# Kernel optimization log

Measured on AMD Instinct MI355X. Metric: run time of the kernel, lower is better.

Reference implementation:

```python
import jax, jax.numpy as jnp
import numpy as np

NUM_OBJECTS = 6          # self.NUM_OBJECTS
SCORE_THRESH = 1e-4      # self.score_tresh
NMS_THRESHS = jnp.asarray(np.arange(0.001, 1.0, 0.1), dtype=jnp.float32)  # 10 thresholds
K_CAND = 1024            # fixed-shape cap on (proposal,class) candidates per image
CLASS_OFFSET = 4096.0    # > max image coord; batched_nms per-class offset trick


def _iou_matrix(b):
    # b: [K,4] xyxy -> [K,K] IoU
    x1, y1, x2, y2 = b[:, 0], b[:, 1], b[:, 2], b[:, 3]
    area = (x2 - x1) * (y2 - y1)
    iw = jnp.clip(jnp.minimum(x2[:, None], x2[None, :]) - jnp.maximum(x1[:, None], x1[None, :]), 0.0)
    ih = jnp.clip(jnp.minimum(y2[:, None], y2[None, :]) - jnp.maximum(y1[:, None], y1[None, :]), 0.0)
    inter = iw * ih
    union = area[:, None] + area[None, :] - inter
    return jnp.where(union > 0, inter / union, 0.0)


def _greedy_nms(iou, valid, thresh):
    # candidates are pre-sorted by descending score; sequential greedy suppression
    K = valid.shape[0]
    ar = jnp.arange(K)
    def body(i, keep):
        sup = keep[i] & (iou[i] > thresh) & (ar > i)
        return keep & ~sup
    return jax.lax.fori_loop(0, K, body, valid)


def _per_image(logits, boxes, feats, hw):
    # logits [N,81], boxes [N,80,4], feats [N,2048], hw [2] (h,w)
    C = boxes.shape[1]
    probs = jax.nn.softmax(logits, axis=-1)[:, :C]          # drop background class
    h = hw[0].astype(boxes.dtype)
    w = hw[1].astype(boxes.dtype)
    b = jnp.stack([jnp.clip(boxes[..., 0], 0.0, w),         # clip to image
                   jnp.clip(boxes[..., 1], 0.0, h),
                   jnp.clip(boxes[..., 2], 0.0, w),
                   jnp.clip(boxes[..., 3], 0.0, h)], axis=-1)
    scores = probs.reshape(-1)                              # [N*C]
    vals, idx = jax.lax.top_k(jnp.where(scores > SCORE_THRESH, scores, -1.0), K_CAND)
    cand_valid = vals > SCORE_THRESH
    cb = b.reshape(-1, 4)[idx]                              # [K,4]
    cls = (idx % C).astype(boxes.dtype)
    prop = idx // C                                         # proposal row index
    iou = _iou_matrix(cb + cls[:, None] * CLASS_OFFSET)     # per-class NMS via offsets
    keeps = jax.vmap(lambda t: _greedy_nms(iou, cand_valid, t))(NMS_THRESHS)  # [T,K]
    counts = keeps.sum(axis=1)
    # torch loop: break at first (smallest) thresh yielding len(ids)==6, i.e. >=6 kept
    ok = counts >= NUM_OBJECTS
    t_sel = jnp.where(jnp.any(ok), jnp.argmax(ok), NMS_THRESHS.shape[0] - 1)
    keep = keeps[t_sel]
    _, top = jax.lax.top_k(jnp.where(keep, vals, -jnp.inf), NUM_OBJECTS)
    ids = prop[top]                                         # [6]
    return feats[ids].T                                     # [2048, 6] (permute(1,0))


def _forward(cls_logits, boxes, feature_pooled, image_hw):
    return jax.vmap(_per_image)(cls_logits, boxes, feature_pooled, image_hw)  # [B,2048,6]


def setup_inputs() -> dict:
    key = jax.random.key(0)
    k1, k2, k3, k4, k5 = jax.random.split(key, 5)
    B, N, C, D = 8, 1000, 80, 2048
    cls_logits = jax.random.normal(k1, (B, N, C + 1), dtype=jnp.float32)
    ctr = jax.random.uniform(k2, (B, N, C, 2), minval=0.0, maxval=800.0)
    sz = jax.random.uniform(k3, (B, N, C, 2), minval=8.0, maxval=200.0)
    boxes = jnp.concatenate([ctr - sz * 0.5, ctr + sz * 0.5], axis=-1).astype(jnp.float32)
    feature_pooled = jax.random.normal(k4, (B, N, D), dtype=jnp.float32)
    image_hw = jax.random.randint(k5, (B, 2), 600, 800, dtype=jnp.int32)
    return {"cls_logits": cls_logits, "boxes": boxes,
            "feature_pooled": feature_pooled, "image_hw": image_hw}


def reference(cls_logits, boxes, feature_pooled, image_hw):
    return _forward(cls_logits, boxes, feature_pooled, image_hw)
```

## Files before the change

kernel.cpp:

```cpp
#include <hip/hip_runtime.h>
#include <cmath>
#include <cstdint>

#define NB 8
#define NPROP 1000
#define NCLS 80
#define NLOG 81
#define KCAND 1024
#define NTH 10
#define DFEAT 2048
#define NOBJ 6
#define NSCORE (NPROP*NCLS)
#define HBLK 8
#define HCHUNK (NSCORE/HBLK)
#define PCHUNK (NPROP/HBLK)
#define CCAP 64

constexpr size_t OFF_SCORES = 0;
constexpr size_t SZ_SCORES  = (size_t)NB * NSCORE * 4;
constexpr size_t OFF_LISTA  = OFF_SCORES + SZ_SCORES;
constexpr size_t SZ_LISTA   = (size_t)NB * 20 * KCAND * 8;
constexpr size_t OFF_H1     = OFF_LISTA;
constexpr size_t OFF_H2     = OFF_H1 + (size_t)NB * HBLK * 2048 * 4;
constexpr size_t OFF_PIV    = OFF_H2 + (size_t)NB * HBLK * 2048 * 4;
constexpr size_t OFF_CBUF   = OFF_PIV + (size_t)NB * 8 * 4;
constexpr size_t OFF_CANDK  = OFF_LISTA + SZ_LISTA;
constexpr size_t SZ_CANDK   = (size_t)NB * KCAND * 8;
constexpr size_t OFF_CX1    = OFF_CANDK + SZ_CANDK;
constexpr size_t SZ_CARR    = (size_t)NB * KCAND * 4;
constexpr size_t OFF_CY1    = OFF_CX1 + SZ_CARR;
constexpr size_t OFF_CX2    = OFF_CY1 + SZ_CARR;
constexpr size_t OFF_CY2    = OFF_CX2 + SZ_CARR;
constexpr size_t OFF_CAREA  = OFF_CY2 + SZ_CARR;
constexpr size_t OFF_CPROP  = OFF_CAREA + SZ_CARR;
constexpr size_t OFF_VALIDW = OFF_CPROP + SZ_CARR;
constexpr size_t SZ_VALIDW  = (size_t)NB * 16 * 8;
constexpr size_t OFF_CCNT   = OFF_VALIDW + SZ_VALIDW;
constexpr size_t OFF_CLIST  = OFF_CCNT + (size_t)NB * NCLS * 4;
constexpr size_t OFF_KEEPS  = OFF_CLIST + (size_t)NB * NCLS * CCAP * 4;
constexpr size_t SZ_KEEPS   = (size_t)NB * NTH * 16 * 8;

__device__ __forceinline__ float nms_th(int t) {
    return (float)(0.001 + 0.1 * (double)t);
}

__device__ __forceinline__ unsigned score_vkey(float v) {
    float vv = (v > 1e-4f) ? v : -1.0f;
    unsigned bits = __float_as_uint(vv);
    unsigned u = (bits & 0x80000000u) ? ~bits : (bits | 0x80000000u);
    return ~u;
}

__global__ __launch_bounds__(1024) void k_softhist(const float* __restrict__ logits,
                                                   float* __restrict__ scores,
                                                   unsigned* __restrict__ hist1) {
    __shared__ unsigned hh[2048];
    int img = blockIdx.x >> 3, blk = blockIdx.x & 7;
    int tid = threadIdx.x, wid = tid >> 6, lane = tid & 63;
    hh[tid] = 0; hh[tid + 1024] = 0;
    __syncthreads();
    for (int p = wid; p < PCHUNK; p += 16) {
        int prop = blk * PCHUNK + p;
        const float* L = logits + ((size_t)img * NPROP + prop) * NLOG;
        float l0 = L[lane];
        float l1 = (lane < 17) ? L[64 + lane] : -INFINITY;
        float m = fmaxf(l0, l1);
        #pragma unroll
        for (int o = 32; o > 0; o >>= 1) m = fmaxf(m, __shfl_xor(m, o, 64));
        float e0 = expf(l0 - m);
        float e1 = (lane < 17) ? expf(l1 - m) : 0.f;
        float s = e0 + e1;
        #pragma unroll
        for (int o = 32; o > 0; o >>= 1) s += __shfl_xor(s, o, 64);
        float* op = scores + ((size_t)img * NPROP + prop) * NCLS;
        float p0 = e0 / s;
        op[lane] = p0;
        atomicAdd(&hh[score_vkey(p0) >> 21], 1u);
        if (lane < 16) {
            float p1 = e1 / s;
            op[64 + lane] = p1;
            atomicAdd(&hh[score_vkey(p1) >> 21], 1u);
        }
    }
    __syncthreads();
    unsigned* outp = hist1 + ((size_t)img * HBLK + blk) * 2048;
    outp[tid] = hh[tid];
    outp[tid + 1024] = hh[tid + 1024];
}

__device__ __forceinline__ void pivot_scan(const unsigned* __restrict__ h8, unsigned K,
                                           int* __restrict__ out_b, int* __restrict__ out_rem) {
    __shared__ unsigned wsum[16];
    int tid = threadIdx.x;
    unsigned a = 0, b = 0;
    #pragma unroll
    for (int s = 0; s < HBLK; ++s) {
        a += h8[s * 2048 + 2 * tid];
        b += h8[s * 2048 + 2 * tid + 1];
    }
    unsigned p = a + b;
    unsigned x = p;
    #pragma unroll
    for (int d = 1; d < 64; d <<= 1) {
        unsigned y = __shfl_up(x, (unsigned)d, 64);
        if ((tid & 63) >= d) x += y;
    }
    if ((tid & 63) == 63) wsum[tid >> 6] = x;
    __syncthreads();
    if (tid < 16) {
        unsigned w = wsum[tid];
        #pragma unroll
        for (int d = 1; d < 16; d <<= 1) {
            unsigned y = __shfl_up(w, (unsigned)d, 64);
            if (tid >= d) w += y;
        }
        wsum[tid] = w;
    }
    __syncthreads();
    unsigned wex = (tid >= 64) ? wsum[(tid >> 6) - 1] : 0u;
    unsigned incl = x + wex;
    unsigned E = incl - p;
    if (E < K && E + a >= K)              { *out_b = 2 * tid;     *out_rem = (int)(K - E); }
    else if (E + a < K && E + a + b >= K) { *out_b = 2 * tid + 1; *out_rem = (int)(K - (E + a)); }
}

__global__ __launch_bounds__(1024) void k_hist2p(const float* __restrict__ scores,
                                                 const unsigned* __restrict__ hist1,
                                                 unsigned* __restrict__ hist2,
                                                 int* __restrict__ piv) {
    __shared__ unsigned hh[2048];
    __shared__ int sb, sr;
    int img = blockIdx.x >> 3, blk = blockIdx.x & 7;
    int tid = threadIdx.x;
    hh[tid] = 0; hh[tid + 1024] = 0;
    pivot_scan(hist1 + (size_t)img * HBLK * 2048, KCAND, &sb, &sr);
    __syncthreads();
    unsigned b1 = (unsigned)sb;
    const float* sc = scores + (size_t)img * NSCORE + (size_t)blk * HCHUNK;
    for (int e = tid; e < HCHUNK; e += 1024) {
        unsigned vk = score_vkey(sc[e]);
        if ((vk >> 21) == b1) atomicAdd(&hh[(vk >> 10) & 2047u], 1u);
    }
    __syncthreads();
    unsigned* outp = hist2 + ((size_t)img * HBLK + blk) * 2048;
    outp[tid] = hh[tid];
    outp[tid + 1024] = hh[tid + 1024];
    if (blk == 0 && tid == 0) {
        piv[img * 8 + 0] = sb;
        piv[img * 8 + 1] = sr;
        piv[img * 8 + 3] = 0;
    }
}

__global__ __launch_bounds__(1024) void k_gatherp(const float* __restrict__ scores,
                                                  const unsigned* __restrict__ hist2,
                                                  int* __restrict__ piv,
                                                  unsigned long long* __restrict__ cbuf,
                                                  int* __restrict__ ccnt,
                                                  unsigned long long* __restrict__ validw,
                                                  unsigned long long* __restrict__ keeps) {
    __shared__ int sb2, sr2;
    __shared__ unsigned lcnt, gbase;
    int img = blockIdx.x >> 3, blk = blockIdx.x & 7;
    int tid = threadIdx.x;
    if (blockIdx.x == 0) {
        if (tid < NB * NCLS) ccnt[tid] = 0;
        if (tid >= 640 && tid < 640 + NB * 16) validw[tid - 640] = 0ULL;
    }
    if (blockIdx.x == 1) {
        for (int k = tid; k < NB * NTH * 16; k += 1024) keeps[k] = 0ULL;
    }
    if (tid == 0) lcnt = 0;
    unsigned K2 = (unsigned)piv[img * 8 + 1];
    pivot_scan(hist2 + (size_t)img * HBLK * 2048, K2, &sb2, &sr2);
    __syncthreads();
    unsigned T22 = ((unsigned)piv[img * 8 + 0] << 11) | (unsigned)sb2;
    const float* sc = scores + (size_t)img * NSCORE + (size_t)blk * HCHUNK;
    unsigned long long sel[(HCHUNK + 1023) / 1024];
    int ns = 0;
    for (int e = tid; e < HCHUNK; e += 1024) {
        unsigned vk = score_vkey(sc[e]);
        if ((vk >> 10) <= T22)
            sel[ns++] = ((unsigned long long)vk << 32) | (unsigned)(blk * HCHUNK + e);
    }
    unsigned lp = atomicAdd(&lcnt, (unsigned)ns);
    __syncthreads();
    if (tid == 0) gbase = atomicAdd((unsigned*)&piv[img * 8 + 3], lcnt);
    __syncthreads();
    unsigned long long* ob = cbuf + (size_t)img * 2048;
    for (int i = 0; i < ns; ++i) {
        unsigned pos = gbase + lp + (unsigned)i;
        if (pos < 2048) ob[pos] = sel[i];
    }
}

__global__ __launch_bounds__(256) void k_rankcand(const unsigned long long* __restrict__ cbuf,
                                                  const int* __restrict__ piv,
                                                  const float* __restrict__ boxes,
                                                  const int* __restrict__ hw,
                                                  float* __restrict__ cx1, float* __restrict__ cy1,
                                                  float* __restrict__ cx2, float* __restrict__ cy2,
                                                  float* __restrict__ car, int* __restrict__ cprop,
                                                  unsigned long long* __restrict__ validw,
                                                  int* __restrict__ ccnt, int* __restrict__ clist) {
    __shared__ unsigned long long keys[2048];
    int img = blockIdx.x >> 3, sl = blockIdx.x & 7;
    int tid = threadIdx.x;
    int cnt = piv[img * 8 + 3]; if (cnt > 2048) cnt = 2048;
    const unsigned long long* ib = cbuf + (size_t)img * 2048;
    #pragma unroll
    for (int k = 0; k < 8; ++k) {
        int t = k * 256 + tid;
        keys[t] = (t < cnt) ? ib[t] : ~0ULL;
    }
    __syncthreads();
    unsigned long long a = keys[sl * 256 + tid];
    int r = 0;
    #pragma unroll 8
    for (int j = 0; j < cnt; ++j) r += (keys[j] < a) ? 1 : 0;
    if (sl * 256 + tid < cnt && r < KCAND) {
        unsigned u   = ~(unsigned)(a >> 32);
        unsigned idx = (unsigned)a;
        const unsigned uth = __float_as_uint(1e-4f) | 0x80000000u;
        bool valid = u > uth;
        int prop = (int)(idx / NCLS);
        int cls  = (int)(idx - (unsigned)prop * NCLS);
        const float4 bx = *(const float4*)(boxes + ((((size_t)img * NPROP + prop) * NCLS + cls) << 2));
        float h = (float)hw[img * 2 + 0];
        float w = (float)hw[img * 2 + 1];
        float x1 = fminf(fmaxf(bx.x, 0.f), w);
        float y1 = fminf(fmaxf(bx.y, 0.f), h);
        float x2 = fminf(fmaxf(bx.z, 0.f), w);
        float y2 = fminf(fmaxf(bx.w, 0.f), h);
        float offc = __fmul_rn((float)cls, 4096.0f);
        x1 = __fadd_rn(x1, offc); y1 = __fadd_rn(y1, offc);
        x2 = __fadd_rn(x2, offc); y2 = __fadd_rn(y2, offc);
        float area = __fmul_rn(__fsub_rn(x2, x1), __fsub_rn(y2, y1));
        int o = img * KCAND + r;
        cx1[o] = x1; cy1[o] = y1; cx2[o] = x2; cy2[o] = y2;
        car[o] = area; cprop[o] = prop;
        if (valid) atomicOr(&validw[img * 16 + (r >> 6)], 1ULL << (r & 63));
        int slot = atomicAdd(&ccnt[img * NCLS + cls], 1);
        if (slot < CCAP) clist[(img * NCLS + cls) * CCAP + slot] = r;
    }
}

__global__ __launch_bounds__(256) void k_cnms(const int* __restrict__ ccnt,
                                              const int* __restrict__ clist,
                                              const float* __restrict__ cx1,
                                              const float* __restrict__ cy1,
                                              const float* __restrict__ cx2,
                                              const float* __restrict__ cy2,
                                              const float* __restrict__ car,
                                              const unsigned long long* __restrict__ validw,
                                              unsigned long long* __restrict__ keeps) {
    int gid  = blockIdx.x * 4 + (threadIdx.x >> 6);
    int lane = threadIdx.x & 63;
    if (gid >= NB * NCLS) return;
    int img = gid / NCLS, cls = gid - img * NCLS;
    int n = ccnt[img * NCLS + cls];
    if (n > CCAP) n = CCAP;
    if (n == 0) return;
    int r = (lane < n) ? clist[(img * NCLS + cls) * CCAP + lane] : 0x7fffffff;
    int pos = 0;
    for (int j = 0; j < n; ++j) {
        int rj = __shfl(r, j, 64);
        pos += (rj < r) ? 1 : 0;
    }
    int srt = 0;
    for (int j = 0; j < n; ++j) {
        int pj = __shfl(pos, j, 64);
        int rj = __shfl(r, j, 64);
        if (pj == lane) srt = rj;
    }
    bool act = lane < n;
    int base = img * KCAND;
    float x1 = 0, y1 = 0, x2 = 0, y2 = 0, ar = 0;
    bool val = false;
    if (act) {
        x1 = cx1[base + srt]; y1 = cy1[base + srt];
        x2 = cx2[base + srt]; y2 = cy2[base + srt]; ar = car[base + srt];
        val = (validw[img * 16 + (srt >> 6)] >> (srt & 63)) & 1ULL;
    }
    unsigned long long m[NTH];
    #pragma unroll
    for (int t = 0; t < NTH; ++t) m[t] = 0ULL;
    for (int b = 0; b < n; ++b) {
        float xj1 = __shfl(x1, b, 64), yj1 = __shfl(y1, b, 64);
        float xj2 = __shfl(x2, b, 64), yj2 = __shfl(y2, b, 64);
        float aj  = __shfl(ar, b, 64);
        float iw = fmaxf(__fsub_rn(fminf(x2, xj2), fmaxf(x1, xj1)), 0.f);
        float ih = fmaxf(__fsub_rn(fminf(y2, yj2), fmaxf(y1, yj1)), 0.f);
        float inter = __fmul_rn(iw, ih);
        float uni   = __fsub_rn(__fadd_rn(ar, aj), inter);
        float iou   = (uni > 0.f) ? __fdiv_rn(inter, uni) : 0.f;
        if (act && b < lane) {
            #pragma unroll
            for (int t = 0; t < NTH; ++t)
                if (iou > nms_th(t)) m[t] |= 1ULL << b;
        }
    }
    unsigned long long vmask = __ballot(act && val);
    for (int t = 0; t < NTH; ++t) {
        unsigned long long keep = vmask;
        for (int it = 0; it <= n; ++it) {
            bool nk = act && val && ((m[t] & keep) == 0ULL);
            unsigned long long nb = __ballot(nk);
            if (nb == keep) break;
            keep = nb;
        }
        if (act && ((keep >> lane) & 1ULL))
            atomicOr(&keeps[((size_t)img * NTH + t) * 16 + (srt >> 6)], 1ULL << (srt & 63));
    }
}

__global__ __launch_bounds__(256) void k_selfeat(const unsigned long long* __restrict__ keeps,
                                                 const int* __restrict__ cprop,
                                                 const float* __restrict__ feats,
                                                 float* __restrict__ outp) {
    __shared__ int scnt[NTH];
    __shared__ unsigned long long skw[16];
    __shared__ int stsel;
    __shared__ int sids[NOBJ];
    int img = blockIdx.x >> 3;
    int tid = threadIdx.x;
    if (tid < NTH) scnt[tid] = 0;
    __syncthreads();
    if (tid < NTH * 16) {
        unsigned long long w = keeps[(size_t)img * NTH * 16 + tid];
        int pc = __popcll(w);
        if (pc) atomicAdd(&scnt[tid >> 4], pc);
    }
    __syncthreads();
    if (tid == 0) {
        int tsel = NTH - 1;
        for (int t = 0; t < NTH; ++t) if (scnt[t] >= NOBJ) { tsel = t; break; }
        stsel = tsel;
    }
    __syncthreads();
    if (tid < 16) skw[tid] = keeps[((size_t)img * NTH + stsel) * 16 + tid];
    __syncthreads();
    if (tid == 0) {
        int got = 0;
        for (int k = 0; k < 16 && got < NOBJ; ++k) {
            unsigned long long x = skw[k];
            while (x && got < NOBJ) {
                int b = __builtin_ctzll(x);
                sids[got++] = cprop[img * KCAND + k * 64 + b];
                x &= x - 1;
            }
        }
        for (int k = 0; k < 16 && got < NOBJ; ++k) {
            unsigned long long x = ~skw[k];
            while (x && got < NOBJ) {
                int b = __builtin_ctzll(x);
                sids[got++] = cprop[img * KCAND + k * 64 + b];
                x &= x - 1;
            }
        }
    }
    __syncthreads();
    int d = (blockIdx.x & 7) * 256 + tid;
    const float* fb = feats + (size_t)img * NPROP * DFEAT;
    float* ob = outp + ((size_t)img * DFEAT + d) * NOBJ;
    #pragma unroll
    for (int s = 0; s < NOBJ; ++s)
        ob[s] = fb[(size_t)sids[s] * DFEAT + d];
}

extern "C" void kernel_launch(void* const* d_in, const int* in_sizes, int n_in,
                              void* d_out, int out_size, void* d_ws, size_t ws_size,
                              hipStream_t stream) {
    const float* logits = (const float*)d_in[0];
    const float* boxes  = (const float*)d_in[1];
    const float* feats  = (const float*)d_in[2];
    const int*   hw     = (const int*)d_in[3];
    float* outp = (float*)d_out;

    char* ws = (char*)d_ws;
    float*              scores = (float*)(ws + OFF_SCORES);
    unsigned*           hist1  = (unsigned*)(ws + OFF_H1);
    unsigned*           hist2  = (unsigned*)(ws + OFF_H2);
    int*                piv    = (int*)(ws + OFF_PIV);
    unsigned long long* cbuf   = (unsigned long long*)(ws + OFF_CBUF);
    float* cx1 = (float*)(ws + OFF_CX1);
    float* cy1 = (float*)(ws + OFF_CY1);
    float* cx2 = (float*)(ws + OFF_CX2);
    float* cy2 = (float*)(ws + OFF_CY2);
    float* car = (float*)(ws + OFF_CAREA);
    int*   cprop = (int*)(ws + OFF_CPROP);
    unsigned long long* validw = (unsigned long long*)(ws + OFF_VALIDW);
    int*   ccnt  = (int*)(ws + OFF_CCNT);
    int*   clist = (int*)(ws + OFF_CLIST);
    unsigned long long* keeps  = (unsigned long long*)(ws + OFF_KEEPS);

    k_softhist<<<NB * HBLK, 1024, 0, stream>>>(logits, scores, hist1);
    k_hist2p<<<NB * HBLK, 1024, 0, stream>>>(scores, hist1, hist2, piv);
    k_gatherp<<<NB * HBLK, 1024, 0, stream>>>(scores, hist2, piv, cbuf, ccnt, validw, keeps);
    k_rankcand<<<NB * HBLK, 256, 0, stream>>>(cbuf, piv, boxes, hw,
                                              cx1, cy1, cx2, cy2, car, cprop,
                                              validw, ccnt, clist);
    k_cnms<<<(NB * NCLS + 3) / 4, 256, 0, stream>>>(ccnt, clist, cx1, cy1, cx2, cy2,
                                                    car, validw, keeps);
    k_selfeat<<<NB * HBLK, 256, 0, stream>>>(keeps, cprop, feats, outp);
}
```

Measured before the change: 163.6 us.

## Fuse pivot, gather, sort, NMS and feature select into one per-image kernel

Five kernels after the softmax/histogram pass are merged into a single kernel with one 1024-thread block per image. Candidates, boxes, per-class lists and keep masks now live in shared memory, and the O(n^2) rank sort is replaced by an in-LDS bitonic sort of 2048 keys. The goal is to remove four launches and their global-memory round trips. In exchange, only 8 blocks run, so each block scans the whole 80000-score array twice, and every image's NMS and feature copy run serially within one CU.

```diff
diff --git a/kernel.cpp b/kernel.cpp
--- a/kernel.cpp
+++ b/kernel.cpp
@@ -12,33 +12,12 @@
 #define NOBJ 6
 #define NSCORE (NPROP*NCLS)
 #define HBLK 8
-#define HCHUNK (NSCORE/HBLK)
 #define PCHUNK (NPROP/HBLK)
 #define CCAP 64
 
 constexpr size_t OFF_SCORES = 0;
 constexpr size_t SZ_SCORES  = (size_t)NB * NSCORE * 4;
-constexpr size_t OFF_LISTA  = OFF_SCORES + SZ_SCORES;
-constexpr size_t SZ_LISTA   = (size_t)NB * 20 * KCAND * 8;
-constexpr size_t OFF_H1     = OFF_LISTA;
-constexpr size_t OFF_H2     = OFF_H1 + (size_t)NB * HBLK * 2048 * 4;
-constexpr size_t OFF_PIV    = OFF_H2 + (size_t)NB * HBLK * 2048 * 4;
-constexpr size_t OFF_CBUF   = OFF_PIV + (size_t)NB * 8 * 4;
-constexpr size_t OFF_CANDK  = OFF_LISTA + SZ_LISTA;
-constexpr size_t SZ_CANDK   = (size_t)NB * KCAND * 8;
-constexpr size_t OFF_CX1    = OFF_CANDK + SZ_CANDK;
-constexpr size_t SZ_CARR    = (size_t)NB * KCAND * 4;
-constexpr size_t OFF_CY1    = OFF_CX1 + SZ_CARR;
-constexpr size_t OFF_CX2    = OFF_CY1 + SZ_CARR;
-constexpr size_t OFF_CY2    = OFF_CX2 + SZ_CARR;
-constexpr size_t OFF_CAREA  = OFF_CY2 + SZ_CARR;
-constexpr size_t OFF_CPROP  = OFF_CAREA + SZ_CARR;
-constexpr size_t OFF_VALIDW = OFF_CPROP + SZ_CARR;
-constexpr size_t SZ_VALIDW  = (size_t)NB * 16 * 8;
-constexpr size_t OFF_CCNT   = OFF_VALIDW + SZ_VALIDW;
-constexpr size_t OFF_CLIST  = OFF_CCNT + (size_t)NB * NCLS * 4;
-constexpr size_t OFF_KEEPS  = OFF_CLIST + (size_t)NB * NCLS * CCAP * 4;
-constexpr size_t SZ_KEEPS   = (size_t)NB * NTH * 16 * 8;
+constexpr size_t OFF_H1     = OFF_SCORES + SZ_SCORES;
 
 __device__ __forceinline__ float nms_th(int t) {
     return (float)(0.001 + 0.1 * (double)t);
@@ -88,16 +67,11 @@
     outp[tid + 1024] = hh[tid + 1024];
 }
 
-__device__ __forceinline__ void pivot_scan(const unsigned* __restrict__ h8, unsigned K,
-                                           int* __restrict__ out_b, int* __restrict__ out_rem) {
-    __shared__ unsigned wsum[16];
+__device__ __forceinline__ void pivot_lds(const unsigned* __restrict__ h, unsigned K,
+                                          int* __restrict__ out_b, int* __restrict__ out_rem,
+                                          unsigned* __restrict__ wsum) {
     int tid = threadIdx.x;
-    unsigned a = 0, b = 0;
-    #pragma unroll
-    for (int s = 0; s < HBLK; ++s) {
-        a += h8[s * 2048 + 2 * tid];
-        b += h8[s * 2048 + 2 * tid + 1];
-    }
+    unsigned a = h[2 * tid], b = h[2 * tid + 1];
     unsigned p = a + b;
     unsigned x = p;
     #pragma unroll
@@ -118,217 +92,198 @@
     }
     __syncthreads();
     unsigned wex = (tid >= 64) ? wsum[(tid >> 6) - 1] : 0u;
-    unsigned incl = x + wex;
-    unsigned E = incl - p;
+    unsigned E = x + wex - p;
     if (E < K && E + a >= K)              { *out_b = 2 * tid;     *out_rem = (int)(K - E); }
     else if (E + a < K && E + a + b >= K) { *out_b = 2 * tid + 1; *out_rem = (int)(K - (E + a)); }
 }
 
-__global__ __launch_bounds__(1024) void k_hist2p(const float* __restrict__ scores,
-                                                 const unsigned* __restrict__ hist1,
-                                                 unsigned* __restrict__ hist2,
-                                                 int* __restrict__ piv) {
-    __shared__ unsigned hh[2048];
-    __shared__ int sb, sr;
-    int img = blockIdx.x >> 3, blk = blockIdx.x & 7;
-    int tid = threadIdx.x;
-    hh[tid] = 0; hh[tid + 1024] = 0;
-    pivot_scan(hist1 + (size_t)img * HBLK * 2048, KCAND, &sb, &sr);
-    __syncthreads();
-    unsigned b1 = (unsigned)sb;
-    const float* sc = scores + (size_t)img * NSCORE + (size_t)blk * HCHUNK;
-    for (int e = tid; e < HCHUNK; e += 1024) {
+__global__ __launch_bounds__(1024) void k_mega2(const float* __restrict__ scores,
+                                                const unsigned* __restrict__ hist1,
+                                                const float* __restrict__ boxes,
+                                                const int* __restrict__ hw,
+                                                const float* __restrict__ feats,
+                                                float* __restrict__ outp) {
+    __shared__ __align__(16) unsigned char smem[51200];
+    unsigned*           hist  = (unsigned*)(smem);
+    unsigned long long* keys  = (unsigned long long*)(smem);
+    int*                clist = (int*)(smem);
+    float* bx1 = (float*)(smem + 24576);
+    float* by1 = (float*)(smem + 28672);
+    float* bx2 = (float*)(smem + 32768);
+    float* by2 = (float*)(smem + 36864);
+    float* bar = (float*)(smem + 40960);
+    int*   bprop = (int*)(smem + 45056);
+    unsigned long long* bvalid = (unsigned long long*)(smem + 49152);
+    int*   ccnt  = (int*)(smem + 49280);
+    unsigned long long* keep10 = (unsigned long long*)(smem + 49600);
+    int*   scnt  = (int*)(smem + 50880);
+    __shared__ unsigned wsum[16];
+    __shared__ int sb1, sr1, sb2, sr2, stsel;
+    __shared__ int sids[NOBJ];
+    __shared__ unsigned scounter;
+
+    const int img = blockIdx.x;
+    const int tid = threadIdx.x;
+    const int wv  = tid >> 6, lane = tid & 63;
+    const float* sc = scores + (size_t)img * NSCORE;
+
+    {
+        const unsigned* h8 = hist1 + (size_t)img * HBLK * 2048;
+        unsigned s0 = 0, s1 = 0;
+        #pragma unroll
+        for (int s = 0; s < HBLK; ++s) {
+            s0 += h8[s * 2048 + tid];
+            s1 += h8[s * 2048 + tid + 1024];
+        }
+        hist[tid] = s0; hist[tid + 1024] = s1;
+    }
+    __syncthreads();
+    pivot_lds(hist, KCAND, &sb1, &sr1, wsum);
+    __syncthreads();
+    int b1 = sb1, rem1 = sr1;
+
+    hist[tid] = 0; hist[tid + 1024] = 0;
+    __syncthreads();
+    for (int e = tid; e < NSCORE; e += 1024) {
         unsigned vk = score_vkey(sc[e]);
-        if ((vk >> 21) == b1) atomicAdd(&hh[(vk >> 10) & 2047u], 1u);
-    }
-    __syncthreads();
-    unsigned* outp = hist2 + ((size_t)img * HBLK + blk) * 2048;
-    outp[tid] = hh[tid];
-    outp[tid + 1024] = hh[tid + 1024];
-    if (blk == 0 && tid == 0) {
-        piv[img * 8 + 0] = sb;
-        piv[img * 8 + 1] = sr;
-        piv[img * 8 + 3] = 0;
-    }
-}
-
-__global__ __launch_bounds__(1024) void k_gatherp(const float* __restrict__ scores,
-                                                  const unsigned* __restrict__ hist2,
-                                                  int* __restrict__ piv,
-                                                  unsigned long long* __restrict__ cbuf,
-                                                  int* __restrict__ ccnt,
-                                                  unsigned long long* __restrict__ validw,
-                                                  unsigned long long* __restrict__ keeps) {
-    __shared__ int sb2, sr2;
-    __shared__ unsigned lcnt, gbase;
-    int img = blockIdx.x >> 3, blk = blockIdx.x & 7;
-    int tid = threadIdx.x;
-    if (blockIdx.x == 0) {
-        if (tid < NB * NCLS) ccnt[tid] = 0;
-        if (tid >= 640 && tid < 640 + NB * 16) validw[tid - 640] = 0ULL;
-    }
-    if (blockIdx.x == 1) {
-        for (int k = tid; k < NB * NTH * 16; k += 1024) keeps[k] = 0ULL;
-    }
-    if (tid == 0) lcnt = 0;
-    unsigned K2 = (unsigned)piv[img * 8 + 1];
-    pivot_scan(hist2 + (size_t)img * HBLK * 2048, K2, &sb2, &sr2);
-    __syncthreads();
-    unsigned T22 = ((unsigned)piv[img * 8 + 0] << 11) | (unsigned)sb2;
-    const float* sc = scores + (size_t)img * NSCORE + (size_t)blk * HCHUNK;
-    unsigned long long sel[(HCHUNK + 1023) / 1024];
-    int ns = 0;
-    for (int e = tid; e < HCHUNK; e += 1024) {
+        if ((int)(vk >> 21) == b1) atomicAdd(&hist[(vk >> 10) & 2047u], 1u);
+    }
+    __syncthreads();
+    pivot_lds(hist, (unsigned)rem1, &sb2, &sr2, wsum);
+    __syncthreads();
+    unsigned T22 = ((unsigned)b1 << 11) | (unsigned)sb2;
+
+    __syncthreads();
+    keys[tid] = ~0ULL; keys[tid + 1024] = ~0ULL;
+    if (tid == 0) scounter = 0;
+    __syncthreads();
+    for (int e = tid; e < NSCORE; e += 1024) {
         unsigned vk = score_vkey(sc[e]);
-        if ((vk >> 10) <= T22)
-            sel[ns++] = ((unsigned long long)vk << 32) | (unsigned)(blk * HCHUNK + e);
-    }
-    unsigned lp = atomicAdd(&lcnt, (unsigned)ns);
-    __syncthreads();
-    if (tid == 0) gbase = atomicAdd((unsigned*)&piv[img * 8 + 3], lcnt);
-    __syncthreads();
-    unsigned long long* ob = cbuf + (size_t)img * 2048;
-    for (int i = 0; i < ns; ++i) {
-        unsigned pos = gbase + lp + (unsigned)i;
-        if (pos < 2048) ob[pos] = sel[i];
-    }
-}
-
-__global__ __launch_bounds__(256) void k_rankcand(const unsigned long long* __restrict__ cbuf,
-                                                  const int* __restrict__ piv,
-                                                  const float* __restrict__ boxes,
-                                                  const int* __restrict__ hw,
-                                                  float* __restrict__ cx1, float* __restrict__ cy1,
-                                                  float* __restrict__ cx2, float* __restrict__ cy2,
-                                                  float* __restrict__ car, int* __restrict__ cprop,
-                                                  unsigned long long* __restrict__ validw,
-                                                  int* __restrict__ ccnt, int* __restrict__ clist) {
-    __shared__ unsigned long long keys[2048];
-    int img = blockIdx.x >> 3, sl = blockIdx.x & 7;
-    int tid = threadIdx.x;
-    int cnt = piv[img * 8 + 3]; if (cnt > 2048) cnt = 2048;
-    const unsigned long long* ib = cbuf + (size_t)img * 2048;
-    #pragma unroll
-    for (int k = 0; k < 8; ++k) {
-        int t = k * 256 + tid;
-        keys[t] = (t < cnt) ? ib[t] : ~0ULL;
-    }
-    __syncthreads();
-    unsigned long long a = keys[sl * 256 + tid];
-    int r = 0;
-    #pragma unroll 8
-    for (int j = 0; j < cnt; ++j) r += (keys[j] < a) ? 1 : 0;
-    if (sl * 256 + tid < cnt && r < KCAND) {
-        unsigned u   = ~(unsigned)(a >> 32);
-        unsigned idx = (unsigned)a;
-        const unsigned uth = __float_as_uint(1e-4f) | 0x80000000u;
-        bool valid = u > uth;
-        int prop = (int)(idx / NCLS);
-        int cls  = (int)(idx - (unsigned)prop * NCLS);
-        const float4 bx = *(const float4*)(boxes + ((((size_t)img * NPROP + prop) * NCLS + cls) << 2));
-        float h = (float)hw[img * 2 + 0];
-        float w = (float)hw[img * 2 + 1];
-        float x1 = fminf(fmaxf(bx.x, 0.f), w);
-        float y1 = fminf(fmaxf(bx.y, 0.f), h);
-        float x2 = fminf(fmaxf(bx.z, 0.f), w);
-        float y2 = fminf(fmaxf(bx.w, 0.f), h);
-        float offc = __fmul_rn((float)cls, 4096.0f);
-        x1 = __fadd_rn(x1, offc); y1 = __fadd_rn(y1, offc);
-        x2 = __fadd_rn(x2, offc); y2 = __fadd_rn(y2, offc);
-        float area = __fmul_rn(__fsub_rn(x2, x1), __fsub_rn(y2, y1));
-        int o = img * KCAND + r;
-        cx1[o] = x1; cy1[o] = y1; cx2[o] = x2; cy2[o] = y2;
-        car[o] = area; cprop[o] = prop;
-        if (valid) atomicOr(&validw[img * 16 + (r >> 6)], 1ULL << (r & 63));
-        int slot = atomicAdd(&ccnt[img * NCLS + cls], 1);
-        if (slot < CCAP) clist[(img * NCLS + cls) * CCAP + slot] = r;
-    }
-}
-
-__global__ __launch_bounds__(256) void k_cnms(const int* __restrict__ ccnt,
-                                              const int* __restrict__ clist,
-                                              const float* __restrict__ cx1,
-                                              const float* __restrict__ cy1,
-                                              const float* __restrict__ cx2,
-                                              const float* __restrict__ cy2,
-                                              const float* __restrict__ car,
-                                              const unsigned long long* __restrict__ validw,
-                                              unsigned long long* __restrict__ keeps) {
-    int gid  = blockIdx.x * 4 + (threadIdx.x >> 6);
-    int lane = threadIdx.x & 63;
-    if (gid >= NB * NCLS) return;
-    int img = gid / NCLS, cls = gid - img * NCLS;
-    int n = ccnt[img * NCLS + cls];
-    if (n > CCAP) n = CCAP;
-    if (n == 0) return;
-    int r = (lane < n) ? clist[(img * NCLS + cls) * CCAP + lane] : 0x7fffffff;
-    int pos = 0;
-    for (int j = 0; j < n; ++j) {
-        int rj = __shfl(r, j, 64);
-        pos += (rj < r) ? 1 : 0;
-    }
-    int srt = 0;
-    for (int j = 0; j < n; ++j) {
-        int pj = __shfl(pos, j, 64);
-        int rj = __shfl(r, j, 64);
-        if (pj == lane) srt = rj;
-    }
-    bool act = lane < n;
-    int base = img * KCAND;
-    float x1 = 0, y1 = 0, x2 = 0, y2 = 0, ar = 0;
-    bool val = false;
-    if (act) {
-        x1 = cx1[base + srt]; y1 = cy1[base + srt];
-        x2 = cx2[base + srt]; y2 = cy2[base + srt]; ar = car[base + srt];
-        val = (validw[img * 16 + (srt >> 6)] >> (srt & 63)) & 1ULL;
-    }
-    unsigned long long m[NTH];
-    #pragma unroll
-    for (int t = 0; t < NTH; ++t) m[t] = 0ULL;
-    for (int b = 0; b < n; ++b) {
-        float xj1 = __shfl(x1, b, 64), yj1 = __shfl(y1, b, 64);
-        float xj2 = __shfl(x2, b, 64), yj2 = __shfl(y2, b, 64);
-        float aj  = __shfl(ar, b, 64);
-        float iw = fmaxf(__fsub_rn(fminf(x2, xj2), fmaxf(x1, xj1)), 0.f);
-        float ih = fmaxf(__fsub_rn(fminf(y2, yj2), fmaxf(y1, yj1)), 0.f);
-        float inter = __fmul_rn(iw, ih);
-        float uni   = __fsub_rn(__fadd_rn(ar, aj), inter);
-        float iou   = (uni > 0.f) ? __fdiv_rn(inter, uni) : 0.f;
-        if (act && b < lane) {
+        if ((vk >> 10) <= T22) {
+            unsigned pos = atomicAdd(&scounter, 1u);
+            if (pos < 2048) keys[pos] = ((unsigned long long)vk << 32) | (unsigned)e;
+        }
+    }
+    __syncthreads();
+    int cnt = (int)scounter; if (cnt > 2048) cnt = 2048;
+
+    for (int k = 2; k <= 2048; k <<= 1) {
+        for (int j = k >> 1; j > 0; j >>= 1) {
             #pragma unroll
-            for (int t = 0; t < NTH; ++t)
-                if (iou > nms_th(t)) m[t] |= 1ULL << b;
-        }
-    }
-    unsigned long long vmask = __ballot(act && val);
-    for (int t = 0; t < NTH; ++t) {
-        unsigned long long keep = vmask;
-        for (int it = 0; it <= n; ++it) {
-            bool nk = act && val && ((m[t] & keep) == 0ULL);
-            unsigned long long nb = __ballot(nk);
-            if (nb == keep) break;
-            keep = nb;
-        }
-        if (act && ((keep >> lane) & 1ULL))
-            atomicOr(&keeps[((size_t)img * NTH + t) * 16 + (srt >> 6)], 1ULL << (srt & 63));
-    }
-}
-
-__global__ __launch_bounds__(256) void k_selfeat(const unsigned long long* __restrict__ keeps,
-                                                 const int* __restrict__ cprop,
-                                                 const float* __restrict__ feats,
-                                                 float* __restrict__ outp) {
-    __shared__ int scnt[NTH];
-    __shared__ unsigned long long skw[16];
-    __shared__ int stsel;
-    __shared__ int sids[NOBJ];
-    int img = blockIdx.x >> 3;
-    int tid = threadIdx.x;
+            for (int s = 0; s < 2; ++s) {
+                int i = s * 1024 + tid;
+                int ixj = i ^ j;
+                if (ixj > i) {
+                    bool up = ((i & k) == 0);
+                    unsigned long long a = keys[i], b = keys[ixj];
+                    if ((a > b) == up) { keys[i] = b; keys[ixj] = a; }
+                }
+            }
+            __syncthreads();
+        }
+    }
+
+    int mycls = -1;
+    {
+        bool have = (tid < KCAND) && (tid < cnt);
+        unsigned long long a = have ? keys[tid] : ~0ULL;
+        bool valid = false;
+        if (have) {
+            unsigned u   = ~(unsigned)(a >> 32);
+            unsigned idx = (unsigned)a;
+            const unsigned uth = __float_as_uint(1e-4f) | 0x80000000u;
+            valid = u > uth;
+            int prop = (int)(idx / NCLS);
+            int cls  = (int)(idx - (unsigned)prop * NCLS);
+            mycls = cls;
+            const float4 bx = *(const float4*)(boxes + ((((size_t)img * NPROP + prop) * NCLS + cls) << 2));
+            float h = (float)hw[img * 2 + 0];
+            float w = (float)hw[img * 2 + 1];
+            float x1 = fminf(fmaxf(bx.x, 0.f), w);
+            float y1 = fminf(fmaxf(bx.y, 0.f), h);
+            float x2 = fminf(fmaxf(bx.z, 0.f), w);
+            float y2 = fminf(fmaxf(bx.w, 0.f), h);
+            float offc = __fmul_rn((float)cls, 4096.0f);
+            x1 = __fadd_rn(x1, offc); y1 = __fadd_rn(y1, offc);
+            x2 = __fadd_rn(x2, offc); y2 = __fadd_rn(y2, offc);
+            float area = __fmul_rn(__fsub_rn(x2, x1), __fsub_rn(y2, y1));
+            bx1[tid] = x1; by1[tid] = y1; bx2[tid] = x2; by2[tid] = y2;
+            bar[tid] = area; bprop[tid] = prop;
+        }
+        unsigned long long bal = __ballot(valid);
+        if (tid < KCAND && lane == 0) bvalid[wv] = bal;
+    }
+    __syncthreads();
+
+    if (tid < NCLS) ccnt[tid] = 0;
+    if (tid < NTH * 16) keep10[tid] = 0ULL;
+    __syncthreads();
+    if (mycls >= 0) {
+        int slot = atomicAdd(&ccnt[mycls], 1);
+        if (slot < CCAP) clist[mycls * CCAP + slot] = tid;
+    }
+    __syncthreads();
+
+    for (int cl = wv; cl < NCLS; cl += 16) {
+        int n = ccnt[cl];
+        if (n > CCAP) n = CCAP;
+        if (n == 0) continue;
+        int r = (lane < n) ? clist[cl * CCAP + lane] : 0x7fffffff;
+        int pos = 0;
+        for (int j = 0; j < n; ++j) {
+            int rj = __shfl(r, j, 64);
+            pos += (rj < r) ? 1 : 0;
+        }
+        int srt = 0;
+        for (int j = 0; j < n; ++j) {
+            int pj = __shfl(pos, j, 64);
+            int rj = __shfl(r, j, 64);
+            if (pj == lane) srt = rj;
+        }
+        bool act = lane < n;
+        float x1 = 0, y1 = 0, x2 = 0, y2 = 0, ar = 0;
+        bool val = false;
+        if (act) {
+            x1 = bx1[srt]; y1 = by1[srt]; x2 = bx2[srt]; y2 = by2[srt]; ar = bar[srt];
+            val = (bvalid[srt >> 6] >> (srt & 63)) & 1ULL;
+        }
+        unsigned long long m[NTH];
+        #pragma unroll
+        for (int t = 0; t < NTH; ++t) m[t] = 0ULL;
+        for (int b = 0; b < n; ++b) {
+            float xj1 = __shfl(x1, b, 64), yj1 = __shfl(y1, b, 64);
+            float xj2 = __shfl(x2, b, 64), yj2 = __shfl(y2, b, 64);
+            float aj  = __shfl(ar, b, 64);
+            float iw = fmaxf(__fsub_rn(fminf(x2, xj2), fmaxf(x1, xj1)), 0.f);
+            float ih = fmaxf(__fsub_rn(fminf(y2, yj2), fmaxf(y1, yj1)), 0.f);
+            float inter = __fmul_rn(iw, ih);
+            float uni   = __fsub_rn(__fadd_rn(ar, aj), inter);
+            float iou   = (uni > 0.f) ? __fdiv_rn(inter, uni) : 0.f;
+            if (act && b < lane) {
+                #pragma unroll
+                for (int t = 0; t < NTH; ++t)
+                    if (iou > nms_th(t)) m[t] |= 1ULL << b;
+            }
+        }
+        unsigned long long vmask = __ballot(act && val);
+        for (int t = 0; t < NTH; ++t) {
+            unsigned long long keep = vmask;
+            for (int it = 0; it <= n; ++it) {
+                bool nk = act && val && ((m[t] & keep) == 0ULL);
+                unsigned long long nb = __ballot(nk);
+                if (nb == keep) break;
+                keep = nb;
+            }
+            if (act && ((keep >> lane) & 1ULL))
+                atomicOr(&keep10[t * 16 + (srt >> 6)], 1ULL << (srt & 63));
+        }
+    }
+    __syncthreads();
+
     if (tid < NTH) scnt[tid] = 0;
     __syncthreads();
     if (tid < NTH * 16) {
-        unsigned long long w = keeps[(size_t)img * NTH * 16 + tid];
-        int pc = __popcll(w);
+        int pc = __popcll(keep10[tid]);
         if (pc) atomicAdd(&scnt[tid >> 4], pc);
     }
     __syncthreads();
@@ -336,36 +291,36 @@
         int tsel = NTH - 1;
         for (int t = 0; t < NTH; ++t) if (scnt[t] >= NOBJ) { tsel = t; break; }
         stsel = tsel;
-    }
-    __syncthreads();
-    if (tid < 16) skw[tid] = keeps[((size_t)img * NTH + stsel) * 16 + tid];
-    __syncthreads();
-    if (tid == 0) {
         int got = 0;
+        const unsigned long long* kw = &keep10[tsel * 16];
         for (int k = 0; k < 16 && got < NOBJ; ++k) {
-            unsigned long long x = skw[k];
+            unsigned long long x = kw[k];
             while (x && got < NOBJ) {
                 int b = __builtin_ctzll(x);
-                sids[got++] = cprop[img * KCAND + k * 64 + b];
+                sids[got++] = bprop[k * 64 + b];
                 x &= x - 1;
             }
         }
         for (int k = 0; k < 16 && got < NOBJ; ++k) {
-            unsigned long long x = ~skw[k];
+            unsigned long long x = ~kw[k];
             while (x && got < NOBJ) {
                 int b = __builtin_ctzll(x);
-                sids[got++] = cprop[img * KCAND + k * 64 + b];
+                sids[got++] = bprop[k * 64 + b];
                 x &= x - 1;
             }
         }
     }
     __syncthreads();
-    int d = (blockIdx.x & 7) * 256 + tid;
+
     const float* fb = feats + (size_t)img * NPROP * DFEAT;
-    float* ob = outp + ((size_t)img * DFEAT + d) * NOBJ;
     #pragma unroll
-    for (int s = 0; s < NOBJ; ++s)
-        ob[s] = fb[(size_t)sids[s] * DFEAT + d];
+    for (int rep = 0; rep < 2; ++rep) {
+        int d = rep * 1024 + tid;
+        float* ob = outp + ((size_t)img * DFEAT + d) * NOBJ;
+        #pragma unroll
+        for (int s = 0; s < NOBJ; ++s)
+            ob[s] = fb[(size_t)sids[s] * DFEAT + d];
+    }
 }
 
 extern "C" void kernel_launch(void* const* d_in, const int* in_sizes, int n_in,
@@ -378,29 +333,9 @@
     float* outp = (float*)d_out;
 
     char* ws = (char*)d_ws;
-    float*              scores = (float*)(ws + OFF_SCORES);
-    unsigned*           hist1  = (unsigned*)(ws + OFF_H1);
-    unsigned*           hist2  = (unsigned*)(ws + OFF_H2);
-    int*                piv    = (int*)(ws + OFF_PIV);
-    unsigned long long* cbuf   = (unsigned long long*)(ws + OFF_CBUF);
-    float* cx1 = (float*)(ws + OFF_CX1);
-    float* cy1 = (float*)(ws + OFF_CY1);
-    float* cx2 = (float*)(ws + OFF_CX2);
-    float* cy2 = (float*)(ws + OFF_CY2);
-    float* car = (float*)(ws + OFF_CAREA);
-    int*   cprop = (int*)(ws + OFF_CPROP);
-    unsigned long long* validw = (unsigned long long*)(ws + OFF_VALIDW);
-    int*   ccnt  = (int*)(ws + OFF_CCNT);
-    int*   clist = (int*)(ws + OFF_CLIST);
-    unsigned long long* keeps  = (unsigned long long*)(ws + OFF_KEEPS);
+    float*    scores = (float*)(ws + OFF_SCORES);
+    unsigned* hist1  = (unsigned*)(ws + OFF_H1);
 
     k_softhist<<<NB * HBLK, 1024, 0, stream>>>(logits, scores, hist1);
-    k_hist2p<<<NB * HBLK, 1024, 0, stream>>>(scores, hist1, hist2, piv);
-    k_gatherp<<<NB * HBLK, 1024, 0, stream>>>(scores, hist2, piv, cbuf, ccnt, validw, keeps);
-    k_rankcand<<<NB * HBLK, 256, 0, stream>>>(cbuf, piv, boxes, hw,
-                                              cx1, cy1, cx2, cy2, car, cprop,
-                                              validw, ccnt, clist);
-    k_cnms<<<(NB * NCLS + 3) / 4, 256, 0, stream>>>(ccnt, clist, cx1, cy1, cx2, cy2,
-                                                    car, validw, keeps);
-    k_selfeat<<<NB * HBLK, 256, 0, stream>>>(keeps, cprop, feats, outp);
-}
+    k_mega2<<<NB, 1024, 0, stream>>>(scores, hist1, boxes, hw, feats, outp);
+}
```

Result: slower. 233.2 us (+42.6%).
